# Performance work log

Measured on AMD Instinct MI355X. Metric: run time of the kernel, lower is better.

The kernel has to match this reference:

```python
import jax, jax.numpy as jnp
import numpy as np

B, T, C, H = 4, 2048, 1024, 16
D = C // H  # head_dim = 64

def setup_inputs() -> dict:
    key = jax.random.key(0)
    ks = jax.random.split(key, 5)
    scale = 1.0 / np.sqrt(C)
    return {
        "x": jax.random.normal(ks[0], (B, T, C), dtype=jnp.float32),
        "Wq": jax.random.normal(ks[1], (C, C), dtype=jnp.float32) * scale,
        "Wk": jax.random.normal(ks[2], (C, C), dtype=jnp.float32) * scale,
        "Wv": jax.random.normal(ks[3], (C, C), dtype=jnp.float32) * scale,
        "Wo": jax.random.normal(ks[4], (C, C), dtype=jnp.float32) * scale,
        "bo": jnp.zeros((C,), dtype=jnp.float32),
    }

def reference(x, Wq, Wk, Wv, Wo, bo):
    Bx, Tx, Cx = x.shape
    # projections -> [B, H, T, D]
    def split_heads(y):
        return y.reshape(Bx, Tx, H, D).transpose(0, 2, 1, 3)
    Q = split_heads(x @ Wq)
    K = split_heads(x @ Wk)
    V = split_heads(x @ Wv)
    # scaled dot-product with causal mask: [B, H, T, T]
    scores = jnp.einsum('bhqd,bhkd->bhqk', Q, K) / jnp.sqrt(jnp.asarray(D, x.dtype))
    causal = jnp.tril(jnp.ones((Tx, Tx), dtype=bool))
    scores = jnp.where(causal, scores, -jnp.inf)
    weights = jax.nn.softmax(scores, axis=-1)
    attn = jnp.einsum('bhqk,bhkd->bhqd', weights, V)  # [B, H, T, D]
    out = attn.transpose(0, 2, 1, 3).reshape(Bx, Tx, Cx)
    return out @ Wo + bo
```

## Files before the change

### kernel.cpp

```cpp
#include <hip/hip_runtime.h>
#include <hip/hip_bf16.h>
#include <cmath>

typedef __bf16 bf16;
typedef __bf16 bf16x8 __attribute__((ext_vector_type(8)));
typedef __bf16 bf16x4v __attribute__((ext_vector_type(4)));
typedef float f32x4 __attribute__((ext_vector_type(4)));

#define B_ 4
#define T_ 2048
#define C_ 1024
#define H_ 16
#define D_ 64
#define BT_ 8192
#define LOG2E 1.4426950408889634f

__device__ __forceinline__ void async_cp16(const void* g, void* l) {
  __builtin_amdgcn_global_load_lds(
      (__attribute__((address_space(1))) void*)g,
      (__attribute__((address_space(3))) void*)l, 16, 0, 0);
}

__device__ __forceinline__ f32x4 mfma16(bf16x8 a, bf16x8 b, f32x4 c) {
  return __builtin_amdgcn_mfma_f32_16x16x32_bf16(a, b, c, 0, 0, 0);
}

__global__ __launch_bounds__(256) void prep_kernel(
    const float* __restrict__ x, const float* __restrict__ Wq,
    const float* __restrict__ Wk, const float* __restrict__ Wv,
    const float* __restrict__ Wo, bf16* __restrict__ xb,
    bf16* __restrict__ wt) {
  __shared__ float tile[32][33];
  const int id = blockIdx.x;
  const int t = threadIdx.x;
  if (id < 8192) {
    const int i = id * 256 + t;
    float4 v = ((const float4*)x)[i];
    bf16x4v o = {(bf16)v.x, (bf16)v.y, (bf16)v.z, (bf16)v.w};
    ((bf16x4v*)xb)[i] = o;
    return;
  }
  const int id2 = id - 8192;
  const int z = id2 >> 10;
  const float* W = (z == 0) ? Wq : (z == 1) ? Wk : (z == 2) ? Wv : Wo;
  bf16* Wt = wt + (size_t)z * 1048576;
  const int bx = id2 & 31, by = (id2 >> 5) & 31;
  const int xx = t & 31, yy = t >> 5;
  const int n0 = bx * 32, k0 = by * 32;
#pragma unroll
  for (int j = 0; j < 32; j += 8)
    tile[yy + j][xx] = W[(size_t)(k0 + yy + j) * C_ + n0 + xx];
  __syncthreads();
#pragma unroll
  for (int j = 0; j < 32; j += 8)
    Wt[(size_t)(n0 + yy + j) * C_ + k0 + xx] = (bf16)tile[xx][yy + j];
}

template <int F32OUT>
__device__ __forceinline__ void gemm_tile_sb(
    const bf16* __restrict__ A, const bf16* __restrict__ Bt,
    void* __restrict__ Cv, const float* __restrict__ bias, int M, int N, int K,
    int m0, int n0, bf16* As, bf16* Bs) {
  const int t = threadIdx.x;
  const int lane = t & 63;
  const int wave = t >> 6;
  const int quad = lane >> 4;
  const int l15 = lane & 15;
  const int l7 = l15 & 7;
  const int wm = (wave >> 1) * 64;
  const int wn = (wave & 1) * 64;

  const int sr8 = lane >> 3;
  const int sc = (lane & 7) ^ sr8;
  const bf16* Ag = A + (size_t)(m0 + wave * 32 + sr8) * K + sc * 8;
  const bf16* Bg = Bt + (size_t)(n0 + wave * 32 + sr8) * K + sc * 8;

  const int niter = K >> 6;
  auto stage = [&](int kt) {
    bf16* Ad = As + wave * 2048 + lane * 8;
    bf16* Bd = Bs + wave * 2048 + lane * 8;
#pragma unroll
    for (int i = 0; i < 4; i++) {
      async_cp16(Ag + kt * 64 + (size_t)(i * 8) * K, Ad + i * 512);
      async_cp16(Bg + kt * 64 + (size_t)(i * 8) * K, Bd + i * 512);
    }
  };

  f32x4 acc[4][4] = {};

  for (int kt = 0; kt < niter; kt++) {
    if (kt) __syncthreads();
    stage(kt);
    __syncthreads();
#pragma unroll
    for (int ks = 0; ks < 2; ks++) {
      bf16x8 af[4], bfr[4];
#pragma unroll
      for (int i = 0; i < 4; i++)
        af[i] = *(const bf16x8*)&As[(wm + i * 16 + l15) * 64 +
                                    (((ks * 4 + quad) ^ l7) * 8)];
#pragma unroll
      for (int j = 0; j < 4; j++)
        bfr[j] = *(const bf16x8*)&Bs[(wn + j * 16 + l15) * 64 +
                                     (((ks * 4 + quad) ^ l7) * 8)];
#pragma unroll
      for (int i = 0; i < 4; i++)
#pragma unroll
        for (int j = 0; j < 4; j++)
          acc[i][j] = mfma16(af[i], bfr[j], acc[i][j]);
    }
  }

#pragma unroll
  for (int i = 0; i < 4; i++) {
    const int gr = m0 + wm + i * 16 + quad * 4;
#pragma unroll
    for (int j = 0; j < 4; j++) {
      const int gc = n0 + wn + j * 16 + l15;
      const float bv = F32OUT ? bias[gc] : 0.0f;
#pragma unroll
      for (int r = 0; r < 4; r++) {
        const float v = acc[i][j][r] + bv;
        if (F32OUT)
          ((float*)Cv)[(size_t)(gr + r) * N + gc] = v;
        else
          ((bf16*)Cv)[(size_t)(gr + r) * N + gc] = (bf16)v;
      }
    }
  }
}

__global__ __launch_bounds__(256, 4) void qkv_gemm_kernel(
    const bf16* __restrict__ xb, const bf16* __restrict__ wqkvT,
    bf16* __restrict__ qkb, bf16* __restrict__ vtb) {
  __shared__ __align__(16) bf16 As[8192];
  __shared__ __align__(16) bf16 Bs[8192];
  int id = blockIdx.x;
  if (id < 1024) {
    gemm_tile_sb<0>(xb, wqkvT, (void*)qkb, nullptr, 8192, 2048, 1024,
                    (id >> 4) * 128, (id & 15) * 128, As, Bs);
  } else {
    id -= 1024;
    gemm_tile_sb<0>(wqkvT + 2 * 1024 * 1024, xb, (void*)vtb, nullptr, 1024,
                    8192, 1024, (id >> 6) * 128, (id & 63) * 128, As, Bs);
  }
}

__global__ __launch_bounds__(256, 4) void out_gemm_kernel(
    const bf16* __restrict__ attn, const bf16* __restrict__ woT,
    float* __restrict__ out, const float* __restrict__ bo) {
  __shared__ __align__(16) bf16 As[8192];
  __shared__ __align__(16) bf16 Bs[8192];
  const int id = blockIdx.x;
  gemm_tile_sb<1>(attn, woT, (void*)out, bo, 8192, 1024, 1024,
                  (id >> 3) * 128, (id & 7) * 128, As, Bs);
}

__global__ __launch_bounds__(256, 3) void flash_attn_kernel(
    const bf16* __restrict__ qk, const bf16* __restrict__ vt,
    bf16* __restrict__ attn) {
  __shared__ __align__(16) char smem[51200];
  bf16* KsB = (bf16*)smem;
  bf16* VsB = (bf16*)(smem + 16384);
  bf16* Ps = (bf16*)(smem + 32768);

  const int t = threadIdx.x;
  const int lane = t & 63;
  const int wave = t >> 6;
  const int quad = lane >> 4;
  const int l15 = lane & 15;
  const int l7 = l15 & 7;
  const int bx = blockIdx.x;
  const int qt = 15 - (bx >> 6);
  const int bh = bx & 63;
  const int b = bh >> 4;
  const int h = bh & 15;

  const bf16* Qg = qk + (size_t)b * T_ * 2048 + h * 64;
  const bf16* Kg = qk + (size_t)b * T_ * 2048 + 1024 + h * 64;
  const bf16* Vg = vt + (size_t)h * 64 * BT_ + b * T_;

  const float QSCALE = 0.125f * LOG2E;
  bf16x8 qf[2][2];
  const int qrow0 = qt * 128 + wave * 32;
#pragma unroll
  for (int mt = 0; mt < 2; mt++)
#pragma unroll
    for (int ks = 0; ks < 2; ks++) {
      bf16x8 v = *(const bf16x8*)(Qg + (size_t)(qrow0 + mt * 16 + l15) * 2048 +
                                  ks * 32 + quad * 8);
#pragma unroll
      for (int j = 0; j < 8; j++) v[j] = (bf16)((float)v[j] * QSCALE);
      qf[mt][ks] = v;
    }

  f32x4 o_acc[4][2] = {};
  f32x4 l4[2] = {};

  const int sr8 = lane >> 3;
  const int sc = (lane & 7) ^ sr8;

  auto stage = [&](int j64, int buf) {
    const int k0 = j64 * 64;
    bf16* KL = KsB + buf * 4096 + wave * 1024 + lane * 8;
    const bf16* KG = Kg + (size_t)(k0 + wave * 16 + sr8) * 2048 + sc * 8;
    async_cp16(KG, KL);
    async_cp16(KG + (size_t)8 * 2048, KL + 512);
    bf16* VL = VsB + buf * 4096 + wave * 1024 + lane * 8;
    const bf16* VG = Vg + (size_t)(wave * 16 + sr8) * BT_ + k0 + sc * 8;
    async_cp16(VG, VL);
    async_cp16(VG + (size_t)8 * BT_, VL + 512);
  };

  const int S = 2 * qt + 2;
  stage(0, 0);

  for (int s = 0; s < S; s++) {
    __syncthreads();
    if (s + 1 < S) stage(s + 1, (s + 1) & 1);
    const bf16* Kb = KsB + (s & 1) * 4096;
    const bf16* Vb = VsB + (s & 1) * 4096;
    const int k0 = s * 64;
    const bool diag = (s >= 2 * qt);

    bf16x4v p[2][4];
#pragma unroll
    for (int kt = 0; kt < 4; kt++) {
      const bf16x8 kf0 =
          *(const bf16x8*)&Kb[(kt * 16 + l15) * 64 + ((quad ^ l7) * 8)];
      const bf16x8 kf1 =
          *(const bf16x8*)&Kb[(kt * 16 + l15) * 64 + (((4 + quad) ^ l7) * 8)];
#pragma unroll
      for (int mt = 0; mt < 2; mt++) {
        __builtin_amdgcn_s_setprio(1);
        f32x4 sv = mfma16(kf0, qf[mt][0], f32x4{0.f, 0.f, 0.f, 0.f});
        sv = mfma16(kf1, qf[mt][1], sv);
        __builtin_amdgcn_s_setprio(0);
        if (diag) {
          const int qg = qt * 128 + wave * 32 + mt * 16 + l15;
#pragma unroll
          for (int i = 0; i < 4; i++)
            if (k0 + kt * 16 + quad * 4 + i > qg) sv[i] = -INFINITY;
        }
        f32x4 e;
#pragma unroll
        for (int i = 0; i < 4; i++) e[i] = __builtin_amdgcn_exp2f(sv[i]);
        l4[mt] += e;
        p[mt][kt] = bf16x4v{(bf16)e[0], (bf16)e[1], (bf16)e[2], (bf16)e[3]};
      }
    }

#pragma unroll
    for (int mt = 0; mt < 2; mt++) {
      const int row = wave * 32 + mt * 16 + l15;
#pragma unroll
      for (int kt = 0; kt < 4; kt++)
        *(bf16x4v*)&Ps[row * 72 + kt * 16 + quad * 4] = p[mt][kt];
    }

#pragma unroll
    for (int ks2 = 0; ks2 < 2; ks2++) {
      bf16x8 pa[2], vb[4];
#pragma unroll
      for (int mt = 0; mt < 2; mt++)
        pa[mt] = *(const bf16x8*)&Ps[(wave * 32 + mt * 16 + l15) * 72 +
                                     ks2 * 32 + quad * 8];
#pragma unroll
      for (int dt = 0; dt < 4; dt++)
        vb[dt] = *(const bf16x8*)&Vb[(dt * 16 + l15) * 64 +
                                     (((ks2 * 4 + quad) ^ l7) * 8)];
      __builtin_amdgcn_s_setprio(1);
#pragma unroll
      for (int dt = 0; dt < 4; dt++)
#pragma unroll
        for (int mt = 0; mt < 2; mt++)
          o_acc[dt][mt] = mfma16(vb[dt], pa[mt], o_acc[dt][mt]);
      __builtin_amdgcn_s_setprio(0);
    }
  }

  float inv[2];
#pragma unroll
  for (int mt = 0; mt < 2; mt++) {
    float l = l4[mt][0] + l4[mt][1] + l4[mt][2] + l4[mt][3];
    l += __shfl_xor(l, 16, 64);
    l += __shfl_xor(l, 32, 64);
    inv[mt] = 1.0f / l;
  }
#pragma unroll
  for (int dt = 0; dt < 4; dt++)
#pragma unroll
    for (int mt = 0; mt < 2; mt++) {
      const int q = qt * 128 + wave * 32 + mt * 16 + l15;
      bf16x4v o = {(bf16)(o_acc[dt][mt][0] * inv[mt]),
                   (bf16)(o_acc[dt][mt][1] * inv[mt]),
                   (bf16)(o_acc[dt][mt][2] * inv[mt]),
                   (bf16)(o_acc[dt][mt][3] * inv[mt])};
      *(bf16x4v*)(attn + (size_t)(b * T_ + q) * 1024 + h * 64 + dt * 16 +
                  quad * 4) = o;
    }
}

extern "C" void kernel_launch(void* const* d_in, const int* in_sizes, int n_in,
                              void* d_out, int out_size, void* d_ws,
                              size_t ws_size, hipStream_t stream) {
  const float* x = (const float*)d_in[0];
  const float* Wq = (const float*)d_in[1];
  const float* Wk = (const float*)d_in[2];
  const float* Wv = (const float*)d_in[3];
  const float* Wo = (const float*)d_in[4];
  const float* bo = (const float*)d_in[5];
  float* out = (float*)d_out;

  char* ws = (char*)d_ws;
  bf16* xb = (bf16*)(ws);
  bf16* qkb = (bf16*)(ws + 16777216);
  bf16* vtb = (bf16*)(ws + 50331648);
  bf16* attn = (bf16*)(ws + 67108864);
  bf16* wqkvT = (bf16*)(ws + 83886080);

  prep_kernel<<<12288, 256, 0, stream>>>(x, Wq, Wk, Wv, Wo, xb, wqkvT);

  qkv_gemm_kernel<<<1536, 256, 0, stream>>>(xb, wqkvT, qkb, vtb);

  flash_attn_kernel<<<1024, 256, 0, stream>>>(qkb, vtb, attn);

  out_gemm_kernel<<<512, 256, 0, stream>>>(attn, wqkvT + 3 * 1024 * 1024, out,
                                           bo);
}
```

Before: 237.2 us.

## Double-buffer out-proj GEMM, single-buffer attention for occupancy, permute q-tile order

After: 235.6 us. No clear change (-0.7%).

```diff
diff --git a/kernel.cpp b/kernel.cpp
--- a/kernel.cpp
+++ b/kernel.cpp
@@ -130,6 +130,82 @@
   }
 }
 
+template <int F32OUT>
+__device__ __forceinline__ void gemm_tile_db(
+    const bf16* __restrict__ A, const bf16* __restrict__ Bt,
+    void* __restrict__ Cv, const float* __restrict__ bias, int M, int N, int K,
+    int m0, int n0, bf16* As, bf16* Bs) {
+  const int t = threadIdx.x;
+  const int lane = t & 63;
+  const int wave = t >> 6;
+  const int quad = lane >> 4;
+  const int l15 = lane & 15;
+  const int l7 = l15 & 7;
+  const int wm = (wave >> 1) * 64;
+  const int wn = (wave & 1) * 64;
+
+  const int sr8 = lane >> 3;
+  const int sc = (lane & 7) ^ sr8;
+  const bf16* Ag = A + (size_t)(m0 + wave * 32 + sr8) * K + sc * 8;
+  const bf16* Bg = Bt + (size_t)(n0 + wave * 32 + sr8) * K + sc * 8;
+
+  const int niter = K >> 6;
+  auto stage = [&](int kt, int buf) {
+    bf16* Ad = As + buf * 8192 + wave * 2048 + lane * 8;
+    bf16* Bd = Bs + buf * 8192 + wave * 2048 + lane * 8;
+#pragma unroll
+    for (int i = 0; i < 4; i++) {
+      async_cp16(Ag + kt * 64 + (size_t)(i * 8) * K, Ad + i * 512);
+      async_cp16(Bg + kt * 64 + (size_t)(i * 8) * K, Bd + i * 512);
+    }
+  };
+
+  f32x4 acc[4][4] = {};
+  stage(0, 0);
+
+  for (int kt = 0; kt < niter; kt++) {
+    __syncthreads();
+    if (kt + 1 < niter) stage(kt + 1, (kt + 1) & 1);
+    const bf16* Ab = As + (kt & 1) * 8192;
+    const bf16* Bb = Bs + (kt & 1) * 8192;
+#pragma unroll
+    for (int ks = 0; ks < 2; ks++) {
+      bf16x8 af[4], bfr[4];
+#pragma unroll
+      for (int i = 0; i < 4; i++)
+        af[i] = *(const bf16x8*)&Ab[(wm + i * 16 + l15) * 64 +
+                                    (((ks * 4 + quad) ^ l7) * 8)];
+#pragma unroll
+      for (int j = 0; j < 4; j++)
+        bfr[j] = *(const bf16x8*)&Bb[(wn + j * 16 + l15) * 64 +
+                                     (((ks * 4 + quad) ^ l7) * 8)];
+#pragma unroll
+      for (int i = 0; i < 4; i++)
+#pragma unroll
+        for (int j = 0; j < 4; j++)
+          acc[i][j] = mfma16(af[i], bfr[j], acc[i][j]);
+    }
+  }
+
+#pragma unroll
+  for (int i = 0; i < 4; i++) {
+    const int gr = m0 + wm + i * 16 + quad * 4;
+#pragma unroll
+    for (int j = 0; j < 4; j++) {
+      const int gc = n0 + wn + j * 16 + l15;
+      const float bv = F32OUT ? bias[gc] : 0.0f;
+#pragma unroll
+      for (int r = 0; r < 4; r++) {
+        const float v = acc[i][j][r] + bv;
+        if (F32OUT)
+          ((float*)Cv)[(size_t)(gr + r) * N + gc] = v;
+        else
+          ((bf16*)Cv)[(size_t)(gr + r) * N + gc] = (bf16)v;
+      }
+    }
+  }
+}
+
 __global__ __launch_bounds__(256, 4) void qkv_gemm_kernel(
     const bf16* __restrict__ xb, const bf16* __restrict__ wqkvT,
     bf16* __restrict__ qkb, bf16* __restrict__ vtb) {
@@ -146,23 +222,26 @@
   }
 }
 
-__global__ __launch_bounds__(256, 4) void out_gemm_kernel(
+__global__ __launch_bounds__(256, 2) void out_gemm_kernel(
     const bf16* __restrict__ attn, const bf16* __restrict__ woT,
     float* __restrict__ out, const float* __restrict__ bo) {
-  __shared__ __align__(16) bf16 As[8192];
-  __shared__ __align__(16) bf16 Bs[8192];
+  __shared__ __align__(16) bf16 As[2 * 8192];
+  __shared__ __align__(16) bf16 Bs[2 * 8192];
   const int id = blockIdx.x;
-  gemm_tile_sb<1>(attn, woT, (void*)out, bo, 8192, 1024, 1024,
+  gemm_tile_db<1>(attn, woT, (void*)out, bo, 8192, 1024, 1024,
                   (id >> 3) * 128, (id & 7) * 128, As, Bs);
 }
 
-__global__ __launch_bounds__(256, 3) void flash_attn_kernel(
+__constant__ int QTPERM[16] = {15, 14, 13, 12, 8, 9, 10, 11,
+                               7,  6,  5,  4,  0, 1, 2,  3};
+
+__global__ __launch_bounds__(256, 4) void flash_attn_kernel(
     const bf16* __restrict__ qk, const bf16* __restrict__ vt,
     bf16* __restrict__ attn) {
-  __shared__ __align__(16) char smem[51200];
-  bf16* KsB = (bf16*)smem;
-  bf16* VsB = (bf16*)(smem + 16384);
-  bf16* Ps = (bf16*)(smem + 32768);
+  __shared__ __align__(16) char smem[34816];
+  bf16* Ks = (bf16*)smem;
+  bf16* Vs = (bf16*)(smem + 8192);
+  bf16* Ps = (bf16*)(smem + 16384);
 
   const int t = threadIdx.x;
   const int lane = t & 63;
@@ -171,7 +250,7 @@
   const int l15 = lane & 15;
   const int l7 = l15 & 7;
   const int bx = blockIdx.x;
-  const int qt = 15 - (bx >> 6);
+  const int qt = QTPERM[bx >> 6];
   const int bh = bx & 63;
   const int b = bh >> 4;
   const int h = bh & 15;
@@ -200,26 +279,24 @@
   const int sr8 = lane >> 3;
   const int sc = (lane & 7) ^ sr8;
 
-  auto stage = [&](int j64, int buf) {
+  auto stage = [&](int j64) {
     const int k0 = j64 * 64;
-    bf16* KL = KsB + buf * 4096 + wave * 1024 + lane * 8;
+    bf16* KL = Ks + wave * 1024 + lane * 8;
     const bf16* KG = Kg + (size_t)(k0 + wave * 16 + sr8) * 2048 + sc * 8;
     async_cp16(KG, KL);
     async_cp16(KG + (size_t)8 * 2048, KL + 512);
-    bf16* VL = VsB + buf * 4096 + wave * 1024 + lane * 8;
+    bf16* VL = Vs + wave * 1024 + lane * 8;
     const bf16* VG = Vg + (size_t)(wave * 16 + sr8) * BT_ + k0 + sc * 8;
     async_cp16(VG, VL);
     async_cp16(VG + (size_t)8 * BT_, VL + 512);
   };
 
   const int S = 2 * qt + 2;
-  stage(0, 0);
 
   for (int s = 0; s < S; s++) {
+    if (s) __syncthreads();
+    stage(s);
     __syncthreads();
-    if (s + 1 < S) stage(s + 1, (s + 1) & 1);
-    const bf16* Kb = KsB + (s & 1) * 4096;
-    const bf16* Vb = VsB + (s & 1) * 4096;
     const int k0 = s * 64;
     const bool diag = (s >= 2 * qt);
 
@@ -227,9 +304,9 @@
 #pragma unroll
     for (int kt = 0; kt < 4; kt++) {
       const bf16x8 kf0 =
-          *(const bf16x8*)&Kb[(kt * 16 + l15) * 64 + ((quad ^ l7) * 8)];
+          *(const bf16x8*)&Ks[(kt * 16 + l15) * 64 + ((quad ^ l7) * 8)];
       const bf16x8 kf1 =
-          *(const bf16x8*)&Kb[(kt * 16 + l15) * 64 + (((4 + quad) ^ l7) * 8)];
+          *(const bf16x8*)&Ks[(kt * 16 + l15) * 64 + (((4 + quad) ^ l7) * 8)];
 #pragma unroll
       for (int mt = 0; mt < 2; mt++) {
         __builtin_amdgcn_s_setprio(1);
@@ -267,7 +344,7 @@
                                      ks2 * 32 + quad * 8];
 #pragma unroll
       for (int dt = 0; dt < 4; dt++)
-        vb[dt] = *(const bf16x8*)&Vb[(dt * 16 + l15) * 64 +
+        vb[dt] = *(const bf16x8*)&Vs[(dt * 16 + l15) * 64 +
                                      (((ks2 * 4 + quad) ^ l7) * 8)];
       __builtin_amdgcn_s_setprio(1);
 #pragma unroll
```
